# Performance work log

Hardware: AMD Instinct MI355X
Metric: run time of the kernel (lower is better)

Reference implementation:

```python
import jax, jax.numpy as jnp
import numpy as np

NUM_TREES = 64
INPUT_DIM = 512
DEPTH = 6
NUM_CLASSES = 10
INIT_TEMP = 2.0
SHRINKAGE = 0.3
BN_EPS = 1e-5
ATTN_HIDDEN = 128


def setup_inputs() -> dict:
    key = jax.random.key(0)
    ks = jax.random.split(key, 10)
    B = 16384
    num_nodes = 2 ** DEPTH - 1   # 63
    num_leaves = 2 ** DEPTH      # 64
    x = jax.random.normal(ks[0], (B, INPUT_DIM), dtype=jnp.float32)
    # Attention network params (Linear stored as [in, out])
    attn_w1 = jax.random.normal(ks[1], (INPUT_DIM, ATTN_HIDDEN), dtype=jnp.float32) / np.sqrt(INPUT_DIM)
    attn_b1 = jnp.zeros((ATTN_HIDDEN,), jnp.float32)
    bn_gamma = jnp.ones((ATTN_HIDDEN,), jnp.float32)
    bn_beta = jnp.zeros((ATTN_HIDDEN,), jnp.float32)
    bn_mean = jnp.zeros((ATTN_HIDDEN,), jnp.float32)   # eval-mode running stats
    bn_var = jnp.ones((ATTN_HIDDEN,), jnp.float32)
    attn_w2 = jax.random.normal(ks[2], (ATTN_HIDDEN, NUM_TREES), dtype=jnp.float32) / np.sqrt(ATTN_HIDDEN)
    attn_b2 = jnp.zeros((NUM_TREES,), jnp.float32)
    # Stacked per-tree params
    tree_w = jax.random.normal(ks[3], (NUM_TREES, num_nodes, INPUT_DIM), dtype=jnp.float32)
    tree_b = jnp.zeros((NUM_TREES, num_nodes), jnp.float32)
    tree_temp = jnp.full((NUM_TREES,), INIT_TEMP, jnp.float32)
    leaf_values = jax.random.normal(ks[4], (NUM_TREES, num_leaves, NUM_CLASSES), dtype=jnp.float32)
    residual_weights = jax.nn.sigmoid(jax.random.normal(ks[5], (NUM_TREES,), dtype=jnp.float32))
    return {
        'x': x, 'attn_w1': attn_w1, 'attn_b1': attn_b1,
        'bn_gamma': bn_gamma, 'bn_beta': bn_beta, 'bn_mean': bn_mean, 'bn_var': bn_var,
        'attn_w2': attn_w2, 'attn_b2': attn_b2,
        'tree_w': tree_w, 'tree_b': tree_b, 'tree_temp': tree_temp,
        'leaf_values': leaf_values, 'residual_weights': residual_weights,
    }


def _forward(x, attn_w1, attn_b1, bn_gamma, bn_beta, bn_mean, bn_var,
             attn_w2, attn_b2, tree_w, tree_b, tree_temp, leaf_values, residual_weights):
    # --- attention weights over trees ---
    h = jax.nn.relu(x @ attn_w1 + attn_b1)
    h = (h - bn_mean) * jax.lax.rsqrt(bn_var + BN_EPS) * bn_gamma + bn_beta  # BatchNorm1d eval
    attn = jax.nn.softmax(h @ attn_w2 + attn_b2, axis=1)  # [B, T]

    # --- soft-tree ensemble (eval mode: no dropout, no tree skipping) ---
    missing = jnp.isnan(x)
    xc = jnp.where(missing, 0.0, x)
    missing_any = jnp.any(missing, axis=1)  # [B]

    # All split logits in one GEMM: [B, T, num_nodes]
    logits = jnp.einsum('bd,tnd->btn', xc, tree_w) + tree_b[None]
    dec = jax.nn.sigmoid(logits / tree_temp[None, :, None])
    dec = jnp.where(missing_any[:, None, None], 0.5, dec)

    B, T = x.shape[0], tree_w.shape[0]
    routing = jnp.ones((B, T, 1), x.dtype)
    for lvl in range(DEPTH):
        d = dec[:, :, 2 ** lvl - 1: 2 ** (lvl + 1) - 1]  # [B, T, 2^lvl]
        # matches torch: routing.repeat(1,2) * cat([d, 1-d])
        routing = jnp.concatenate([routing, routing], -1) * jnp.concatenate([d, 1.0 - d], -1)
    # routing now [B, T, 2^DEPTH] = leaf probabilities

    tree_out = jnp.einsum('btl,tlc->btc', routing, leaf_values)  # [B, T, C]
    coef = SHRINKAGE * residual_weights  # [T]
    pred = jnp.einsum('bt,t,btc->bc', attn, coef, tree_out)
    return jax.nn.softmax(pred, axis=1)  # multiclass_classification


def reference(x, attn_w1, attn_b1, bn_gamma, bn_beta, bn_mean, bn_var,
              attn_w2, attn_b2, tree_w, tree_b, tree_temp, leaf_values, residual_weights):
    return _forward(x, attn_w1, attn_b1, bn_gamma, bn_beta, bn_mean, bn_var,
                    attn_w2, attn_b2, tree_w, tree_b, tree_temp, leaf_values, residual_weights)
```

## Files before the change

### kernel.cpp

```cpp
#include <hip/hip_runtime.h>
#include <hip/hip_fp16.h>
#include <stdint.h>

#define IN_DIM 512
#define NT 64
#define AH 128
#define NCLS 10
#define BN_EPS_C 1e-5f
#define SHRINK 0.3f
#define HSTRIDE 66
#define HPLANE 8448

typedef __bf16 bf16x8 __attribute__((ext_vector_type(8)));
typedef float f32x4 __attribute__((ext_vector_type(4)));
typedef unsigned int u32x4 __attribute__((ext_vector_type(4)));

__device__ __forceinline__ unsigned short f2bf(float f) {
  unsigned u = __builtin_bit_cast(unsigned, f);
  u += 0x7fffu + ((u >> 16) & 1u);
  return (unsigned short)(u >> 16);
}

__device__ __forceinline__ float bflo(unsigned w) {
  return __builtin_bit_cast(float, w << 16);
}
__device__ __forceinline__ float bfhi(unsigned w) {
  return __builtin_bit_cast(float, w & 0xffff0000u);
}

__device__ __forceinline__ void gload_lds16(const void* g, void* l) {
  __builtin_amdgcn_global_load_lds(
      (const __attribute__((address_space(1))) void*)g,
      (__attribute__((address_space(3))) void*)l, 16, 0, 0);
}

__device__ __forceinline__ bf16x8 frag_ld(const char* lds, int r, int q) {
  return *reinterpret_cast<const bf16x8*>(lds + r * 128 + ((q ^ (r & 7)) * 16));
}

__global__ void __launch_bounds__(256) k_prep(
    const float* __restrict__ tw, unsigned short* __restrict__ twb,
    const float* __restrict__ w1, unsigned short* __restrict__ w1t) {
  int b = blockIdx.x;
  if (b < 1024) {
    int tid = b * 256 + threadIdx.x;
    int o = tid * 8;
    int k = o & 511;
    int nt = o >> 9;
    int node = nt & 63, t = nt >> 6;
    union { unsigned short s[8]; u32x4 u; } pk;
    if (node < 63) {
      const float* p = tw + ((t * 63 + node) * 512 + k);
      float4 a = *(const float4*)p, bb = *(const float4*)(p + 4);
      float v[8] = {a.x, a.y, a.z, a.w, bb.x, bb.y, bb.z, bb.w};
#pragma unroll
      for (int i = 0; i < 8; i++) pk.s[i] = f2bf(v[i]);
    } else {
#pragma unroll
      for (int i = 0; i < 8; i++) pk.s[i] = 0;
    }
    *reinterpret_cast<u32x4*>(twb + o) = pk.u;
  } else {
    int tid = (b - 1024) * 256 + threadIdx.x;
    int k = tid & 511, n = tid >> 9;
    w1t[n * 512 + k] = f2bf(w1[k * 128 + n]);
  }
}

__global__ void __launch_bounds__(256) k_attn(
    const float* __restrict__ x, unsigned short* __restrict__ xc,
    float* __restrict__ flags,
    const unsigned short* __restrict__ w1t,
    const float* __restrict__ b1, const float* __restrict__ gam,
    const float* __restrict__ bet, const float* __restrict__ mu,
    const float* __restrict__ var, const float* __restrict__ w2,
    const float* __restrict__ b2, const float* __restrict__ rw,
    float* __restrict__ wbt) {
  __shared__ __align__(16) char smem[59392];
  char* As = smem;
  char* Bs = smem + 8192;
  unsigned short* hb  = (unsigned short*)(smem + 24576);
  unsigned short* w2s = (unsigned short*)(smem + 41984);
  int lane = threadIdx.x & 63, wid = threadIdx.x >> 6;
  int bm0 = blockIdx.x * 64;
  int m = lane & 15, q = lane >> 4;
  int sub = lane >> 3, cpos = lane & 7;

  for (int i = 0; i < 16; ++i) {
    int r = bm0 + wid * 16 + i;
    const float* px = x + (size_t)r * 512 + lane * 8;
    float4 a = *(const float4*)px;
    float4 bb = *(const float4*)(px + 4);
    float v[8] = {a.x, a.y, a.z, a.w, bb.x, bb.y, bb.z, bb.w};
    bool nan_any = false;
    union { unsigned short s[8]; u32x4 u; } pk;
#pragma unroll
    for (int j = 0; j < 8; j++) {
      bool n = (v[j] != v[j]);
      nan_any |= n;
      pk.s[j] = f2bf(n ? 0.f : v[j]);
    }
    *reinterpret_cast<u32x4*>(xc + (size_t)r * 512 + lane * 8) = pk.u;
    unsigned long long bal = __ballot(nan_any);
    if (lane == 0) flags[r] = bal ? 1.f : 0.f;
  }

  for (int i = threadIdx.x; i < AH * NT; i += 256) {
    int k = i >> 6, n = i & 63;
    w2s[n * 136 + k] = f2bf(w2[i]);
  }
  __syncthreads();

  f32x4 acc[8];
#pragma unroll
  for (int j = 0; j < 8; j++) acc[j] = f32x4{0.f, 0.f, 0.f, 0.f};
  const unsigned short* Ag = xc + (size_t)bm0 * 512;

  for (int ko = 0; ko < 8; ++ko) {
    const unsigned short* Ak = Ag + ko * 64;
    const unsigned short* Bk = w1t + ko * 64;
#pragma unroll
    for (int i = 0; i < 2; i++) {
      int seg = wid * 2 + i;
      int r = seg * 8 + sub;
      int cg = cpos ^ (r & 7);
      gload_lds16(Ak + r * 512 + cg * 8, As + seg * 1024);
    }
#pragma unroll
    for (int i = 0; i < 4; i++) {
      int seg = wid * 4 + i;
      int r = seg * 8 + sub;
      int cg = cpos ^ (r & 7);
      gload_lds16(Bk + r * 512 + cg * 8, Bs + seg * 1024);
    }
    __syncthreads();
#pragma unroll
    for (int ks = 0; ks < 2; ++ks) {
      bf16x8 af = frag_ld(As, wid * 16 + m, ks * 4 + q);
#pragma unroll
      for (int ni = 0; ni < 8; ni++) {
        bf16x8 bfr = frag_ld(Bs, ni * 16 + m, ks * 4 + q);
        acc[ni] = __builtin_amdgcn_mfma_f32_16x16x32_bf16(af, bfr, acc[ni], 0, 0, 0);
      }
    }
    __syncthreads();
  }

#pragma unroll
  for (int ni = 0; ni < 8; ni++) {
    int col = ni * 16 + m;
    float bb = b1[col], ga = gam[col], be = bet[col], mm = mu[col];
    float iv = rsqrtf(var[col] + BN_EPS_C);
#pragma unroll
    for (int r4 = 0; r4 < 4; r4++) {
      int rl = wid * 16 + q * 4 + r4;
      float v = acc[ni][r4] + bb;
      v = fmaxf(v, 0.f);
      v = (v - mm) * iv * ga + be;
      hb[rl * 136 + col] = f2bf(v);
    }
  }

  f32x4 acc2[4];
#pragma unroll
  for (int nt = 0; nt < 4; nt++) acc2[nt] = f32x4{0.f, 0.f, 0.f, 0.f};
#pragma unroll
  for (int ks = 0; ks < 4; ++ks) {
    bf16x8 af = *reinterpret_cast<const bf16x8*>(hb + (wid * 16 + m) * 136 + ks * 32 + q * 8);
#pragma unroll
    for (int nt = 0; nt < 4; nt++) {
      bf16x8 bfr = *reinterpret_cast<const bf16x8*>(w2s + (nt * 16 + m) * 136 + ks * 32 + q * 8);
      acc2[nt] = __builtin_amdgcn_mfma_f32_16x16x32_bf16(af, bfr, acc2[nt], 0, 0, 0);
    }
  }

  float b2v[4], cfv[4];
#pragma unroll
  for (int nt = 0; nt < 4; nt++) {
    int col = nt * 16 + m;
    b2v[nt] = b2[col];
    cfv[nt] = SHRINK * rw[col];
  }
#pragma unroll
  for (int reg = 0; reg < 4; ++reg) {
    float s0 = acc2[0][reg] + b2v[0];
    float s1 = acc2[1][reg] + b2v[1];
    float s2 = acc2[2][reg] + b2v[2];
    float s3 = acc2[3][reg] + b2v[3];
    float mx = fmaxf(fmaxf(s0, s1), fmaxf(s2, s3));
#pragma unroll
    for (int o = 1; o < 16; o <<= 1) mx = fmaxf(mx, __shfl_xor(mx, o));
    float e0 = __expf(s0 - mx), e1 = __expf(s1 - mx);
    float e2 = __expf(s2 - mx), e3 = __expf(s3 - mx);
    float sm = e0 + e1 + e2 + e3;
#pragma unroll
    for (int o = 1; o < 16; o <<= 1) sm += __shfl_xor(sm, o);
    float inv = 1.f / sm;
    int row = bm0 + wid * 16 + q * 4 + reg;
    wbt[row * NT + m]      = e0 * inv * cfv[0];
    wbt[row * NT + 16 + m] = e1 * inv * cfv[1];
    wbt[row * NT + 32 + m] = e2 * inv * cfv[2];
    wbt[row * NT + 48 + m] = e3 * inv * cfv[3];
  }
}

__global__ void __launch_bounds__(256) k_trees(
    const unsigned short* __restrict__ xc,
    const unsigned short* __restrict__ twb,
    const float* __restrict__ tree_b,
    const float* __restrict__ tree_temp,
    const float* __restrict__ leaf,
    const float* __restrict__ wbt,
    const float* __restrict__ flags,
    unsigned short* __restrict__ part) {
  __shared__ __align__(16) char smem[33792];
  char* As = smem;
  char* Bs = smem + 16384;
  unsigned short* dh = (unsigned short*)smem;
  int lane = threadIdx.x & 63, wid = threadIdx.x >> 6;
  int bm0 = blockIdx.y * 128;
  int t0 = blockIdx.x * 2;
  int m = lane & 15, q = lane >> 4;
  int sub = lane >> 3, cpos = lane & 7;
  int rA0 = wid * 32 + m;
  int row_l = threadIdx.x & 127;
  int h = __builtin_amdgcn_readfirstlane((int)(threadIdx.x >> 7));
  int grow = bm0 + row_l;

  f32x4 acc[2][8];
#pragma unroll
  for (int i = 0; i < 2; i++)
#pragma unroll
    for (int j = 0; j < 8; j++) acc[i][j] = f32x4{0.f, 0.f, 0.f, 0.f};

  const unsigned short* Ag = xc + (size_t)bm0 * 512;
  const unsigned short* Bg = twb + (size_t)t0 * 64 * 512;

  for (int ko = 0; ko < 8; ++ko) {
    const unsigned short* Ak = Ag + ko * 64;
    const unsigned short* Bk = Bg + ko * 64;
#pragma unroll
    for (int i = 0; i < 4; i++) {
      int seg = wid * 4 + i;
      int r = seg * 8 + sub;
      int cg = cpos ^ (r & 7);
      gload_lds16(Ak + r * 512 + cg * 8, As + seg * 1024);
      gload_lds16(Bk + r * 512 + cg * 8, Bs + seg * 1024);
    }
    __syncthreads();
#pragma unroll
    for (int ks = 0; ks < 2; ++ks) {
      bf16x8 af[2];
#pragma unroll
      for (int mi = 0; mi < 2; mi++) af[mi] = frag_ld(As, rA0 + mi * 16, ks * 4 + q);
#pragma unroll
      for (int ni = 0; ni < 8; ni++) {
        bf16x8 bfr = frag_ld(Bs, ni * 16 + m, ks * 4 + q);
#pragma unroll
        for (int mi = 0; mi < 2; mi++)
          acc[mi][ni] = __builtin_amdgcn_mfma_f32_16x16x32_bf16(af[mi], bfr, acc[mi][ni], 0, 0, 0);
      }
    }
    __syncthreads();
  }

  float flv[2][4];
  {
    float4 f0 = *(const float4*)(flags + bm0 + wid * 32 + q * 4);
    float4 f1 = *(const float4*)(flags + bm0 + wid * 32 + 16 + q * 4);
    flv[0][0] = f0.x; flv[0][1] = f0.y; flv[0][2] = f0.z; flv[0][3] = f0.w;
    flv[1][0] = f1.x; flv[1][1] = f1.y; flv[1][2] = f1.z; flv[1][3] = f1.w;
  }
  float2 wpair = *(const float2*)(wbt + grow * 64 + t0);

#pragma unroll
  for (int tt = 0; tt < 2; ++tt) {
    int t = t0 + tt;
    float nk2 = -1.44269504089f / tree_temp[t];
    float ncb[4];
#pragma unroll
    for (int nl = 0; nl < 4; nl++) {
      int node = nl * 16 + m;
      ncb[nl] = ((node < 63) ? tree_b[t * 63 + node] : 0.f) * nk2;
    }
#pragma unroll
    for (int mi = 0; mi < 2; mi++) {
#pragma unroll
      for (int nl = 0; nl < 4; nl++) {
        int node = nl * 16 + m;
        f32x4 a = acc[mi][tt * 4 + nl];
#pragma unroll
        for (int r4 = 0; r4 < 4; r4++) {
          int row = wid * 32 + mi * 16 + q * 4 + r4;
          float e = exp2f(fmaf(a[r4], nk2, ncb[nl]));
          float sig = __builtin_amdgcn_rcpf(1.f + e);
          unsigned short hv = __half_as_ushort(__float2half(sig));
          hv = (flv[mi][r4] != 0.f) ? (unsigned short)0x3800 : hv;
          dh[tt * HPLANE + row * HSTRIDE + node + 1] = hv;
        }
      }
    }
  }
  __syncthreads();

  float pc[10];
#pragma unroll
  for (int c = 0; c < 10; c++) pc[c] = 0.f;

#pragma unroll
  for (int tt = 0; tt < 2; ++tt) {
    int t = t0 + tt;
    const unsigned short* dr = dh + tt * HPLANE + row_l * HSTRIDE;
    float R[16];
    {
      float d0 = __half2float(__ushort_as_half(dr[1]));
      R[0] = d0;
      R[1] = 1.f - d0;
    }
#pragma unroll
    for (int L = 1; L <= 3; ++L) {
      int half = 1 << L;
#pragma unroll
      for (int g = 0; g < half; g += 2) {
        float2 dd = __half22float2(*reinterpret_cast<const __half2*>(dr + half + g));
        float ra = R[g] * dd.x;
        R[g + half] = R[g] - ra;
        R[g] = ra;
        float rb = R[g + 1] * dd.y;
        R[g + 1 + half] = R[g + 1] - rb;
        R[g + 1] = rb;
      }
    }
#pragma unroll
    for (int p = 0; p < 16; p += 2) {
      float2 dd = __half22float2(*reinterpret_cast<const __half2*>(dr + 16 + p));
      float da = h ? (1.f - dd.x) : dd.x;
      float db = h ? (1.f - dd.y) : dd.y;
      R[p] *= da;
      R[p + 1] *= db;
    }
    float a10[10];
#pragma unroll
    for (int c = 0; c < 10; c++) a10[c] = 0.f;
    const float* Lf = leaf + (size_t)(t * 64 + 16 * h) * 10;
#pragma unroll
    for (int p = 0; p < 16; p += 2) {
      float2 dd = __half22float2(*reinterpret_cast<const __half2*>(dr + 32 + 16 * h + p));
      float rla = R[p] * dd.x, rra = R[p] - rla;
      float rlb = R[p + 1] * dd.y, rrb = R[p + 1] - rlb;
#pragma unroll
      for (int c = 0; c < 10; c++) {
        float s = fmaf(rla, Lf[p * 10 + c], a10[c]);
        s = fmaf(rra, Lf[320 + p * 10 + c], s);
        s = fmaf(rlb, Lf[p * 10 + 10 + c], s);
        a10[c] = fmaf(rrb, Lf[330 + p * 10 + c], s);
      }
    }
    float w = tt ? wpair.y : wpair.x;
#pragma unroll
    for (int c = 0; c < 10; c++) pc[c] = fmaf(w, a10[c], pc[c]);
  }

  __syncthreads();
  float* redbuf = reinterpret_cast<float*>(smem);
  if (h == 1) {
#pragma unroll
    for (int c = 0; c < 10; c++) redbuf[row_l * 10 + c] = pc[c];
  }
  __syncthreads();
  if (h == 0) {
    unsigned short* po = part + ((size_t)grow * 32 + blockIdx.x) * 10;
    unsigned wdw[5];
#pragma unroll
    for (int k = 0; k < 5; k++) {
      unsigned lo = f2bf(pc[2 * k] + redbuf[row_l * 10 + 2 * k]);
      unsigned hi = f2bf(pc[2 * k + 1] + redbuf[row_l * 10 + 2 * k + 1]);
      wdw[k] = lo | (hi << 16);
    }
    unsigned* pu = reinterpret_cast<unsigned*>(po);
#pragma unroll
    for (int k = 0; k < 5; k++) pu[k] = wdw[k];
  }
}

__global__ void __launch_bounds__(128) k_finish(const unsigned short* __restrict__ part,
                                               float* __restrict__ out) {
  int row = blockIdx.x * 128 + threadIdx.x;
  const uint4* pu = reinterpret_cast<const uint4*>(part + (size_t)row * 320);
  float v[10];
#pragma unroll
  for (int c = 0; c < 10; c++) v[c] = 0.f;
#pragma unroll
  for (int ch = 0; ch < 8; ++ch) {
    uint4 w0 = pu[ch * 5 + 0];
    uint4 w1 = pu[ch * 5 + 1];
    uint4 w2 = pu[ch * 5 + 2];
    uint4 w3 = pu[ch * 5 + 3];
    uint4 w4 = pu[ch * 5 + 4];
    unsigned dw[20] = {w0.x, w0.y, w0.z, w0.w, w1.x, w1.y, w1.z, w1.w,
                       w2.x, w2.y, w2.z, w2.w, w3.x, w3.y, w3.z, w3.w,
                       w4.x, w4.y, w4.z, w4.w};
#pragma unroll
    for (int d = 0; d < 20; d++) {
      int k = d % 5;
      v[2 * k] += bflo(dw[d]);
      v[2 * k + 1] += bfhi(dw[d]);
    }
  }
  float mx = -1e30f;
#pragma unroll
  for (int c = 0; c < 10; c++) mx = fmaxf(mx, v[c]);
  float sm = 0.f;
#pragma unroll
  for (int c = 0; c < 10; c++) {
    v[c] = __expf(v[c] - mx);
    sm += v[c];
  }
  float inv = 1.f / sm;
#pragma unroll
  for (int c = 0; c < 10; c++) out[row * 10 + c] = v[c] * inv;
}

extern "C" void kernel_launch(void* const* d_in, const int* in_sizes, int n_in,
                              void* d_out, int out_size, void* d_ws, size_t ws_size,
                              hipStream_t stream) {
  const float* x    = (const float*)d_in[0];
  const float* w1   = (const float*)d_in[1];
  const float* b1   = (const float*)d_in[2];
  const float* gam  = (const float*)d_in[3];
  const float* bet  = (const float*)d_in[4];
  const float* mu   = (const float*)d_in[5];
  const float* var  = (const float*)d_in[6];
  const float* w2   = (const float*)d_in[7];
  const float* b2   = (const float*)d_in[8];
  const float* tw   = (const float*)d_in[9];
  const float* tb   = (const float*)d_in[10];
  const float* temp = (const float*)d_in[11];
  const float* leaf = (const float*)d_in[12];
  const float* rw   = (const float*)d_in[13];
  float* out = (float*)d_out;

  char* ws = (char*)d_ws;
  unsigned short* xc  = (unsigned short*)(ws);
  unsigned short* twb = (unsigned short*)(ws + 16777216);
  unsigned short* w1t = (unsigned short*)(ws + 20971520);
  float* wbt  = (float*)(ws + 21102592);
  float* flg  = (float*)(ws + 25296896);
  unsigned short* part = (unsigned short*)(ws + 25362432);

  k_prep<<<1280, 256, 0, stream>>>(tw, twb, w1, w1t);
  k_attn<<<256, 256, 0, stream>>>(x, xc, flg, w1t, b1, gam, bet, mu, var,
                                  w2, b2, rw, wbt);
  dim3 g2(32, 128);
  k_trees<<<g2, 256, 0, stream>>>(xc, twb, tb, temp, leaf, wbt, flg, part);
  k_finish<<<128, 128, 0, stream>>>(part, out);
}
```

Measured before the change: 264.0 us.

## Double-buffer LDS tiles in attention and tree GEMM loops

```diff
diff --git a/kernel.cpp b/kernel.cpp
--- a/kernel.cpp
+++ b/kernel.cpp
@@ -36,6 +36,40 @@
 
 __device__ __forceinline__ bf16x8 frag_ld(const char* lds, int r, int q) {
   return *reinterpret_cast<const bf16x8*>(lds + r * 128 + ((q ^ (r & 7)) * 16));
+}
+
+__device__ __forceinline__ void stage_trees(const unsigned short* Ak,
+                                            const unsigned short* Bk,
+                                            char* As, char* Bs,
+                                            int wid, int sub, int cpos) {
+#pragma unroll
+  for (int i = 0; i < 4; i++) {
+    int seg = wid * 4 + i;
+    int r = seg * 8 + sub;
+    int cg = cpos ^ (r & 7);
+    gload_lds16(Ak + r * 512 + cg * 8, As + seg * 1024);
+    gload_lds16(Bk + r * 512 + cg * 8, Bs + seg * 1024);
+  }
+}
+
+__device__ __forceinline__ void stage_attn(const unsigned short* Ak,
+                                           const unsigned short* Bk,
+                                           char* As, char* Bs,
+                                           int wid, int sub, int cpos) {
+#pragma unroll
+  for (int i = 0; i < 2; i++) {
+    int seg = wid * 2 + i;
+    int r = seg * 8 + sub;
+    int cg = cpos ^ (r & 7);
+    gload_lds16(Ak + r * 512 + cg * 8, As + seg * 1024);
+  }
+#pragma unroll
+  for (int i = 0; i < 4; i++) {
+    int seg = wid * 4 + i;
+    int r = seg * 8 + sub;
+    int cg = cpos ^ (r & 7);
+    gload_lds16(Bk + r * 512 + cg * 8, Bs + seg * 1024);
+  }
 }
 
 __global__ void __launch_bounds__(256) k_prep(
@@ -76,11 +110,13 @@
     const float* __restrict__ var, const float* __restrict__ w2,
     const float* __restrict__ b2, const float* __restrict__ rw,
     float* __restrict__ wbt) {
-  __shared__ __align__(16) char smem[59392];
-  char* As = smem;
-  char* Bs = smem + 8192;
-  unsigned short* hb  = (unsigned short*)(smem + 24576);
-  unsigned short* w2s = (unsigned short*)(smem + 41984);
+  __shared__ __align__(16) char smem[65536];
+  char* A0 = smem;
+  char* B0 = smem + 8192;
+  char* A1 = smem + 24576;
+  char* B1 = smem + 32768;
+  unsigned short* w2s = (unsigned short*)(smem + 49152);
+  unsigned short* hb  = (unsigned short*)smem;
   int lane = threadIdx.x & 63, wid = threadIdx.x >> 6;
   int bm0 = blockIdx.x * 64;
   int m = lane & 15, q = lane >> 4;
@@ -107,7 +143,7 @@
 
   for (int i = threadIdx.x; i < AH * NT; i += 256) {
     int k = i >> 6, n = i & 63;
-    w2s[n * 136 + k] = f2bf(w2[i]);
+    w2s[n * 128 + k] = f2bf(w2[i]);
   }
   __syncthreads();
 
@@ -116,24 +152,18 @@
   for (int j = 0; j < 8; j++) acc[j] = f32x4{0.f, 0.f, 0.f, 0.f};
   const unsigned short* Ag = xc + (size_t)bm0 * 512;
 
+  stage_attn(Ag, w1t, A0, B0, wid, sub, cpos);
+  __syncthreads();
+
+#pragma unroll
   for (int ko = 0; ko < 8; ++ko) {
-    const unsigned short* Ak = Ag + ko * 64;
-    const unsigned short* Bk = w1t + ko * 64;
-#pragma unroll
-    for (int i = 0; i < 2; i++) {
-      int seg = wid * 2 + i;
-      int r = seg * 8 + sub;
-      int cg = cpos ^ (r & 7);
-      gload_lds16(Ak + r * 512 + cg * 8, As + seg * 1024);
-    }
-#pragma unroll
-    for (int i = 0; i < 4; i++) {
-      int seg = wid * 4 + i;
-      int r = seg * 8 + sub;
-      int cg = cpos ^ (r & 7);
-      gload_lds16(Bk + r * 512 + cg * 8, Bs + seg * 1024);
-    }
-    __syncthreads();
+    char* As = (ko & 1) ? A1 : A0;
+    char* Bs = (ko & 1) ? B1 : B0;
+    if (ko < 7) {
+      char* An = (ko & 1) ? A0 : A1;
+      char* Bn = (ko & 1) ? B0 : B1;
+      stage_attn(Ag + (ko + 1) * 64, w1t + (ko + 1) * 64, An, Bn, wid, sub, cpos);
+    }
 #pragma unroll
     for (int ks = 0; ks < 2; ++ks) {
       bf16x8 af = frag_ld(As, wid * 16 + m, ks * 4 + q);
@@ -169,7 +199,7 @@
     bf16x8 af = *reinterpret_cast<const bf16x8*>(hb + (wid * 16 + m) * 136 + ks * 32 + q * 8);
 #pragma unroll
     for (int nt = 0; nt < 4; nt++) {
-      bf16x8 bfr = *reinterpret_cast<const bf16x8*>(w2s + (nt * 16 + m) * 136 + ks * 32 + q * 8);
+      bf16x8 bfr = *reinterpret_cast<const bf16x8*>(w2s + (nt * 16 + m) * 128 + ks * 32 + q * 8);
       acc2[nt] = __builtin_amdgcn_mfma_f32_16x16x32_bf16(af, bfr, acc2[nt], 0, 0, 0);
     }
   }
@@ -213,9 +243,11 @@
     const float* __restrict__ wbt,
     const float* __restrict__ flags,
     unsigned short* __restrict__ part) {
-  __shared__ __align__(16) char smem[33792];
-  char* As = smem;
-  char* Bs = smem + 16384;
+  __shared__ __align__(16) char smem[65536];
+  char* A0 = smem;
+  char* B0 = smem + 16384;
+  char* A1 = smem + 32768;
+  char* B1 = smem + 49152;
   unsigned short* dh = (unsigned short*)smem;
   int lane = threadIdx.x & 63, wid = threadIdx.x >> 6;
   int bm0 = blockIdx.y * 128;
@@ -236,18 +268,18 @@
   const unsigned short* Ag = xc + (size_t)bm0 * 512;
   const unsigned short* Bg = twb + (size_t)t0 * 64 * 512;
 
+  stage_trees(Ag, Bg, A0, B0, wid, sub, cpos);
+  __syncthreads();
+
+#pragma unroll
   for (int ko = 0; ko < 8; ++ko) {
-    const unsigned short* Ak = Ag + ko * 64;
-    const unsigned short* Bk = Bg + ko * 64;
-#pragma unroll
-    for (int i = 0; i < 4; i++) {
-      int seg = wid * 4 + i;
-      int r = seg * 8 + sub;
-      int cg = cpos ^ (r & 7);
-      gload_lds16(Ak + r * 512 + cg * 8, As + seg * 1024);
-      gload_lds16(Bk + r * 512 + cg * 8, Bs + seg * 1024);
-    }
-    __syncthreads();
+    char* As = (ko & 1) ? A1 : A0;
+    char* Bs = (ko & 1) ? B1 : B0;
+    if (ko < 7) {
+      char* An = (ko & 1) ? A0 : A1;
+      char* Bn = (ko & 1) ? B0 : B1;
+      stage_trees(Ag + (ko + 1) * 64, Bg + (ko + 1) * 64, An, Bn, wid, sub, cpos);
+    }
 #pragma unroll
     for (int ks = 0; ks < 2; ++ks) {
       bf16x8 af[2];
```

New measurement: 249.6 us. -5.5%, faster.

## Double-buffer tree GEMM K-loop and switch to 2x2 warp tiling

Applied to the files above, without the earlier changes.

```diff
diff --git a/kernel.cpp b/kernel.cpp
--- a/kernel.cpp
+++ b/kernel.cpp
@@ -36,6 +36,23 @@
 
 __device__ __forceinline__ bf16x8 frag_ld(const char* lds, int r, int q) {
   return *reinterpret_cast<const bf16x8*>(lds + r * 128 + ((q ^ (r & 7)) * 16));
+}
+
+__device__ __forceinline__ bf16x8 frag_ld32(const char* lds, int r, int q) {
+  return *reinterpret_cast<const bf16x8*>(lds + r * 64 + ((q ^ (r & 3)) * 16));
+}
+
+__device__ __forceinline__ void stage32(const unsigned short* Ak,
+                                        const unsigned short* Bk,
+                                        char* As, char* Bs, int tid) {
+#pragma unroll
+  for (int i = 0; i < 2; i++) {
+    int idx = i * 256 + tid;
+    int r = idx >> 2, c = idx & 3;
+    int cg = c ^ (r & 3);
+    gload_lds16(Ak + r * 512 + cg * 8, As + idx * 16);
+    gload_lds16(Bk + r * 512 + cg * 8, Bs + idx * 16);
+  }
 }
 
 __global__ void __launch_bounds__(256) k_prep(
@@ -214,89 +231,86 @@
     const float* __restrict__ flags,
     unsigned short* __restrict__ part) {
   __shared__ __align__(16) char smem[33792];
-  char* As = smem;
-  char* Bs = smem + 16384;
+  char* A0 = smem;
+  char* B0 = smem + 8192;
+  char* A1 = smem + 16384;
+  char* B1 = smem + 24576;
   unsigned short* dh = (unsigned short*)smem;
   int lane = threadIdx.x & 63, wid = threadIdx.x >> 6;
   int bm0 = blockIdx.y * 128;
   int t0 = blockIdx.x * 2;
   int m = lane & 15, q = lane >> 4;
-  int sub = lane >> 3, cpos = lane & 7;
-  int rA0 = wid * 32 + m;
+  int wr = wid >> 1, wc = wid & 1;
   int row_l = threadIdx.x & 127;
   int h = __builtin_amdgcn_readfirstlane((int)(threadIdx.x >> 7));
   int grow = bm0 + row_l;
-
-  f32x4 acc[2][8];
-#pragma unroll
-  for (int i = 0; i < 2; i++)
-#pragma unroll
-    for (int j = 0; j < 8; j++) acc[i][j] = f32x4{0.f, 0.f, 0.f, 0.f};
+  int tid = threadIdx.x;
+
+  f32x4 acc[4][4];
+#pragma unroll
+  for (int i = 0; i < 4; i++)
+#pragma unroll
+    for (int j = 0; j < 4; j++) acc[i][j] = f32x4{0.f, 0.f, 0.f, 0.f};
 
   const unsigned short* Ag = xc + (size_t)bm0 * 512;
   const unsigned short* Bg = twb + (size_t)t0 * 64 * 512;
 
-  for (int ko = 0; ko < 8; ++ko) {
-    const unsigned short* Ak = Ag + ko * 64;
-    const unsigned short* Bk = Bg + ko * 64;
-#pragma unroll
-    for (int i = 0; i < 4; i++) {
-      int seg = wid * 4 + i;
-      int r = seg * 8 + sub;
-      int cg = cpos ^ (r & 7);
-      gload_lds16(Ak + r * 512 + cg * 8, As + seg * 1024);
-      gload_lds16(Bk + r * 512 + cg * 8, Bs + seg * 1024);
-    }
+  stage32(Ag, Bg, A0, B0, tid);
+  __syncthreads();
+
+#pragma unroll
+  for (int ko = 0; ko < 16; ++ko) {
+    char* As = (ko & 1) ? A1 : A0;
+    char* Bs = (ko & 1) ? B1 : B0;
+    if (ko < 15) {
+      char* An = (ko & 1) ? A0 : A1;
+      char* Bn = (ko & 1) ? B0 : B1;
+      stage32(Ag + (ko + 1) * 32, Bg + (ko + 1) * 32, An, Bn, tid);
+    }
+    bf16x8 af[4], bfr[4];
+#pragma unroll
+    for (int mi = 0; mi < 4; mi++) af[mi] = frag_ld32(As, wr * 64 + mi * 16 + m, q);
+#pragma unroll
+    for (int ni = 0; ni < 4; ni++) bfr[ni] = frag_ld32(Bs, wc * 64 + ni * 16 + m, q);
+#pragma unroll
+    for (int mi = 0; mi < 4; mi++)
+#pragma unroll
+      for (int ni = 0; ni < 4; ni++)
+        acc[mi][ni] = __builtin_amdgcn_mfma_f32_16x16x32_bf16(af[mi], bfr[ni], acc[mi][ni], 0, 0, 0);
     __syncthreads();
-#pragma unroll
-    for (int ks = 0; ks < 2; ++ks) {
-      bf16x8 af[2];
-#pragma unroll
-      for (int mi = 0; mi < 2; mi++) af[mi] = frag_ld(As, rA0 + mi * 16, ks * 4 + q);
-#pragma unroll
-      for (int ni = 0; ni < 8; ni++) {
-        bf16x8 bfr = frag_ld(Bs, ni * 16 + m, ks * 4 + q);
-#pragma unroll
-        for (int mi = 0; mi < 2; mi++)
-          acc[mi][ni] = __builtin_amdgcn_mfma_f32_16x16x32_bf16(af[mi], bfr, acc[mi][ni], 0, 0, 0);
-      }
-    }
-    __syncthreads();
-  }
-
-  float flv[2][4];
+  }
+
+  float flv[4][4];
+#pragma unroll
+  for (int mi = 0; mi < 4; mi++) {
+    float4 f0 = *(const float4*)(flags + bm0 + wr * 64 + mi * 16 + q * 4);
+    flv[mi][0] = f0.x; flv[mi][1] = f0.y; flv[mi][2] = f0.z; flv[mi][3] = f0.w;
+  }
+  float2 wpair = *(const float2*)(wbt + grow * 64 + t0);
+
   {
-    float4 f0 = *(const float4*)(flags + bm0 + wid * 32 + q * 4);
-    float4 f1 = *(const float4*)(flags + bm0 + wid * 32 + 16 + q * 4);
-    flv[0][0] = f0.x; flv[0][1] = f0.y; flv[0][2] = f0.z; flv[0][3] = f0.w;
-    flv[1][0] = f1.x; flv[1][1] = f1.y; flv[1][2] = f1.z; flv[1][3] = f1.w;
-  }
-  float2 wpair = *(const float2*)(wbt + grow * 64 + t0);
-
-#pragma unroll
-  for (int tt = 0; tt < 2; ++tt) {
-    int t = t0 + tt;
+    int t = t0 + wc;
     float nk2 = -1.44269504089f / tree_temp[t];
     float ncb[4];
 #pragma unroll
-    for (int nl = 0; nl < 4; nl++) {
-      int node = nl * 16 + m;
-      ncb[nl] = ((node < 63) ? tree_b[t * 63 + node] : 0.f) * nk2;
-    }
-#pragma unroll
-    for (int mi = 0; mi < 2; mi++) {
-#pragma unroll
-      for (int nl = 0; nl < 4; nl++) {
-        int node = nl * 16 + m;
-        f32x4 a = acc[mi][tt * 4 + nl];
+    for (int ni = 0; ni < 4; ni++) {
+      int node = ni * 16 + m;
+      ncb[ni] = ((node < 63) ? tree_b[t * 63 + node] : 0.f) * nk2;
+    }
+#pragma unroll
+    for (int mi = 0; mi < 4; mi++) {
+#pragma unroll
+      for (int ni = 0; ni < 4; ni++) {
+        int node = ni * 16 + m;
+        f32x4 a = acc[mi][ni];
 #pragma unroll
         for (int r4 = 0; r4 < 4; r4++) {
-          int row = wid * 32 + mi * 16 + q * 4 + r4;
-          float e = exp2f(fmaf(a[r4], nk2, ncb[nl]));
+          int row = wr * 64 + mi * 16 + q * 4 + r4;
+          float e = exp2f(fmaf(a[r4], nk2, ncb[ni]));
           float sig = __builtin_amdgcn_rcpf(1.f + e);
           unsigned short hv = __half_as_ushort(__float2half(sig));
           hv = (flv[mi][r4] != 0.f) ? (unsigned short)0x3800 : hv;
-          dh[tt * HPLANE + row * HSTRIDE + node + 1] = hv;
+          dh[wc * HPLANE + row * HSTRIDE + node + 1] = hv;
         }
       }
     }
```

Result: faster. 244.9 us (-7.2%).
